# Performance work log

Hardware: AMD Instinct MI355X
Metric: run time of the kernel (lower is better)

Reference implementation:

```python
import jax, jax.numpy as jnp
import numpy as np

N_NODES = 50000
N_EDGES = 800000
IN_DIM = 128
HID = 64
ZDIM = 64
N_GRAPHS = 64


def gcn_conv(x, W, b, src, dst, n):
    # PyG GCNConv: add self-loops, symmetric deg^-1/2 normalization,
    # linear transform then gather-scatter aggregation.
    h = x @ W  # [N, out]
    loops = jnp.arange(n, dtype=src.dtype)
    s = jnp.concatenate([src, loops])
    d = jnp.concatenate([dst, loops])
    deg = jnp.zeros((n,), h.dtype).at[d].add(1.0)  # includes self-loops -> >=1
    dinv = jax.lax.rsqrt(deg)
    norm = dinv[s] * dinv[d]  # [E+N]
    msg = h[s] * norm[:, None]  # gather [E+N, out]
    out = jnp.zeros_like(h).at[d].add(msg)  # scatter-add
    return out + b


def mean_pool(h, batch, num_graphs):
    sums = jax.ops.segment_sum(h, batch, num_segments=num_graphs)
    cnt = jax.ops.segment_sum(jnp.ones((h.shape[0],), h.dtype), batch,
                              num_segments=num_graphs)
    return sums / jnp.maximum(cnt, 1.0)[:, None]


def setup_inputs() -> dict:
    key = jax.random.key(0)
    ks = jax.random.split(key, 9)
    x = jax.random.normal(ks[0], (N_NODES, IN_DIM), jnp.float32)
    edge_index = jax.random.randint(ks[1], (2, N_EDGES), 0, N_NODES, jnp.int64 if jax.config.jax_enable_x64 else jnp.int32)
    batch = jnp.sort(jax.random.randint(ks[2], (N_NODES,), 0, N_GRAPHS))
    s1 = 1.0 / np.sqrt(IN_DIM)
    s2 = 1.0 / np.sqrt(HID)
    W1 = jax.random.uniform(ks[3], (IN_DIM, HID), jnp.float32, -s1, s1)
    b1 = jnp.zeros((HID,), jnp.float32)
    Wmu = jax.random.uniform(ks[4], (HID, ZDIM), jnp.float32, -s2, s2)
    bmu = jnp.zeros((ZDIM,), jnp.float32)
    Wsig = jax.random.uniform(ks[5], (HID, ZDIM), jnp.float32, -s2, s2)
    bsig = jnp.zeros((ZDIM,), jnp.float32)
    return {"x": x, "edge_index": edge_index, "batch": batch,
            "num_graphs": N_GRAPHS, "W1": W1, "b1": b1,
            "Wmu": Wmu, "bmu": bmu, "Wsig": Wsig, "bsig": bsig}


def reference(x, edge_index, batch, num_graphs, W1, b1, Wmu, bmu, Wsig, bsig):
    src, dst = edge_index[0], edge_index[1]
    n = x.shape[0]
    h = jax.nn.elu(gcn_conv(x, W1, b1, src, dst, n))
    z_mu = mean_pool(jax.nn.elu(gcn_conv(h, Wmu, bmu, src, dst, n)), batch, num_graphs)
    z_sigma = mean_pool(jax.nn.elu(gcn_conv(h, Wsig, bsig, src, dst, n)), batch, num_graphs)
    return (z_mu, z_sigma)
```

## Files before the change

### kernel.cpp

```cpp
#include <hip/hip_runtime.h>
#include <hip/hip_fp16.h>


#define IN_DIM 128
#define HID 64
#define ZDIM 64
#define N_GRAPHS 64
#define SCAN_B 1024

typedef _Float16 half8 __attribute__((ext_vector_type(8)));
typedef float f32x4 __attribute__((ext_vector_type(4)));

__device__ __forceinline__ float elu1(float x) {
    return x > 0.f ? x : expm1f(x);
}

#define ACC8(RV, MV) do { \
    const __half2* _hp = (const __half2*)&(RV); \
    float2 _f0 = __half22float2(_hp[0]); \
    float2 _f1 = __half22float2(_hp[1]); \
    float2 _f2 = __half22float2(_hp[2]); \
    float2 _f3 = __half22float2(_hp[3]); \
    acc[0] = fmaf((MV), _f0.x, acc[0]); \
    acc[1] = fmaf((MV), _f0.y, acc[1]); \
    acc[2] = fmaf((MV), _f1.x, acc[2]); \
    acc[3] = fmaf((MV), _f1.y, acc[3]); \
    acc[4] = fmaf((MV), _f2.x, acc[4]); \
    acc[5] = fmaf((MV), _f2.y, acc[5]); \
    acc[6] = fmaf((MV), _f3.x, acc[6]); \
    acc[7] = fmaf((MV), _f3.y, acc[7]); \
  } while (0)

__global__ void k_count(const int* __restrict__ dst, int* __restrict__ kc,
                        int* __restrict__ rank, int E) {
    int e = blockIdx.x * blockDim.x + threadIdx.x;
    if (e < E) rank[e] = atomicAdd(&kc[dst[e]], 1);
}

__global__ __launch_bounds__(SCAN_B) void k_scan1(const int* __restrict__ kc,
                                                  int* __restrict__ bsum, int n) {
    __shared__ int wpart[16];
    int tid = threadIdx.x, lane = tid & 63, w = tid >> 6;
    int i = blockIdx.x * SCAN_B + tid;
    int v = (i < n) ? kc[i] : 0;
#pragma unroll
    for (int d = 1; d < 64; d <<= 1) v += __shfl_xor(v, d, 64);
    if (lane == 0) wpart[w] = v;
    __syncthreads();
    if (tid < 16) {
        int t = wpart[tid];
#pragma unroll
        for (int d = 1; d < 16; d <<= 1) t += __shfl_xor(t, d, 64);
        if (tid == 0) bsum[blockIdx.x] = t;
    }
}

__global__ __launch_bounds__(SCAN_B) void k_scan3(const int* __restrict__ kc,
                                                  const int* __restrict__ bsum,
                                                  int* __restrict__ offs,
                                                  float* __restrict__ dinv,
                                                  int n, int nb) {
    __shared__ int wsum[16];
    __shared__ int sbase;
    int tid = threadIdx.x, lane = tid & 63, w = tid >> 6;
    if (tid < 64) {
        int v = (tid < nb) ? bsum[tid] : 0;
        int s = v;
#pragma unroll
        for (int d = 1; d < 64; d <<= 1) {
            int u = __shfl_up(s, d, 64);
            if (tid >= d) s += u;
        }
        if (tid == blockIdx.x) sbase = s - v;
    }
    int i = blockIdx.x * SCAN_B + tid;
    int v = (i < n) ? kc[i] : 0;
    int s = v;
#pragma unroll
    for (int d = 1; d < 64; d <<= 1) {
        int u = __shfl_up(s, d, 64);
        if (lane >= d) s += u;
    }
    if (lane == 63) wsum[w] = s;
    __syncthreads();
    if (tid < 16) {
        int t = wsum[tid];
#pragma unroll
        for (int d = 1; d < 16; d <<= 1) {
            int u = __shfl_up(t, d, 64);
            if (tid >= d) t += u;
        }
        wsum[tid] = t;
    }
    __syncthreads();
    int base = sbase + ((w == 0) ? 0 : wsum[w - 1]);
    if (i < n) {
        offs[i + 1] = base + s;
        dinv[i] = 1.0f / sqrtf(1.0f + (float)v);
        if (i == 0) offs[0] = 0;
    }
}

__global__ void k_fill(const int* __restrict__ src, const int* __restrict__ dst,
                       const int* __restrict__ rank, const int* __restrict__ offs,
                       int* __restrict__ csr, int E) {
    int e = blockIdx.x * blockDim.x + threadIdx.x;
    if (e < E) csr[offs[dst[e]] + rank[e]] = src[e];
}

__global__ void k_wfrag(const float* __restrict__ W1,
                        const float* __restrict__ Wmu,
                        const float* __restrict__ Wsig,
                        __half* __restrict__ F1,
                        __half* __restrict__ Fmu,
                        __half* __restrict__ Fsig) {
    int e = blockIdx.x * 256 + threadIdx.x;
    if (e < 8192) {
        int j = e & 7, l = (e >> 3) & 63, ct = (e >> 9) & 3, ks = e >> 11;
        F1[e] = __float2half(W1[(ks * 32 + ((l >> 4) & 3) * 8 + j) * 64 + ct * 16 + (l & 15)]);
    }
    if (e < 4096) {
        int j = e & 7, l = (e >> 3) & 63, ct = (e >> 9) & 3, ks = e >> 11;
        int widx = (ks * 32 + ((l >> 4) & 3) * 8 + j) * 64 + ct * 16 + (l & 15);
        Fmu[e] = __float2half(Wmu[widx]);
        Fsig[e] = __float2half(Wsig[widx]);
    }
}

__global__ __launch_bounds__(256) void k_mm1(const float* __restrict__ x,
                                             const __half* __restrict__ F1,
                                             const float* __restrict__ dinv,
                                             __half* __restrict__ ts1h, int n) {
    int l = threadIdx.x & 63;
    int wave = threadIdx.x >> 6;
    int m0 = blockIdx.x * 64 + wave * 16;
    int row_a = m0 + (l & 15);
    if (row_a >= n) row_a = n - 1;
    int kg = l >> 4;

    f32x4 acc0 = {0.f, 0.f, 0.f, 0.f};
    f32x4 acc1 = acc0, acc2 = acc0, acc3 = acc0;

    const float* xr = x + (size_t)row_a * IN_DIM + kg * 8;
#pragma unroll
    for (int ks = 0; ks < 4; ++ks) {
        float4 xa = *(const float4*)(xr + ks * 32);
        float4 xb = *(const float4*)(xr + ks * 32 + 4);
        half8 a;
        a[0] = (_Float16)xa.x; a[1] = (_Float16)xa.y;
        a[2] = (_Float16)xa.z; a[3] = (_Float16)xa.w;
        a[4] = (_Float16)xb.x; a[5] = (_Float16)xb.y;
        a[6] = (_Float16)xb.z; a[7] = (_Float16)xb.w;
        const __half* fb = F1 + ((size_t)(ks * 4) * 64 + l) * 8;
        half8 b0 = *(const half8*)(fb);
        half8 b1 = *(const half8*)(fb + 512);
        half8 b2 = *(const half8*)(fb + 1024);
        half8 b3 = *(const half8*)(fb + 1536);
        acc0 = __builtin_amdgcn_mfma_f32_16x16x32_f16(a, b0, acc0, 0, 0, 0);
        acc1 = __builtin_amdgcn_mfma_f32_16x16x32_f16(a, b1, acc1, 0, 0, 0);
        acc2 = __builtin_amdgcn_mfma_f32_16x16x32_f16(a, b2, acc2, 0, 0, 0);
        acc3 = __builtin_amdgcn_mfma_f32_16x16x32_f16(a, b3, acc3, 0, 0, 0);
    }
    int col = l & 15;
#pragma unroll
    for (int r = 0; r < 4; ++r) {
        int row = m0 + kg * 4 + r;
        if (row < n) {
            float di = dinv[row];
            __half* p = &ts1h[(size_t)row * 64 + col];
            p[0]  = __float2half(acc0[r] * di);
            p[16] = __float2half(acc1[r] * di);
            p[32] = __float2half(acc2[r] * di);
            p[48] = __float2half(acc3[r] * di);
        }
    }
}

__global__ __launch_bounds__(256) void k_gather_hh(const int* __restrict__ off,
                                                   const int* __restrict__ csr,
                                                   const float* __restrict__ dinv,
                                                   const __half* __restrict__ ts,
                                                   const float* __restrict__ b1,
                                                   __half* __restrict__ hh, int n) {
    int node = blockIdx.x * 4 + (threadIdx.x >> 6);
    if (node >= n) return;
    int lane = threadIdx.x & 63;
    int g = lane >> 3, sub = lane & 7;
    int s0 = off[node], s1 = off[node + 1];
    float acc[8];
#pragma unroll
    for (int j = 0; j < 8; ++j) acc[j] = 0.f;

    if (s1 > s0) {
        int last = s1 - 1;
        int p0 = s0 + g, p1 = p0 + 8, p2 = p0 + 16, p3 = p0 + 24;
        int i0 = csr[p0 < s1 ? p0 : last];
        int i1 = csr[p1 < s1 ? p1 : last];
        int i2 = csr[p2 < s1 ? p2 : last];
        int i3 = csr[p3 < s1 ? p3 : last];
        float4 r0 = *(const float4*)&ts[(size_t)i0 * 64 + sub * 8];
        float4 r1 = *(const float4*)&ts[(size_t)i1 * 64 + sub * 8];
        float4 r2 = *(const float4*)&ts[(size_t)i2 * 64 + sub * 8];
        float4 r3 = *(const float4*)&ts[(size_t)i3 * 64 + sub * 8];
        float m0 = (p0 < s1) ? 1.f : 0.f;
        float m1 = (p1 < s1) ? 1.f : 0.f;
        float m2 = (p2 < s1) ? 1.f : 0.f;
        float m3 = (p3 < s1) ? 1.f : 0.f;
        ACC8(r0, m0);
        ACC8(r1, m1);
        ACC8(r2, m2);
        ACC8(r3, m3);
        for (int k = s0 + 32 + g; k < s1; k += 8) {
            int iv = csr[k];
            float4 rv = *(const float4*)&ts[(size_t)iv * 64 + sub * 8];
            ACC8(rv, 1.f);
        }
    }

#pragma unroll
    for (int j = 0; j < 8; ++j) {
        acc[j] += __shfl_xor(acc[j], 8, 64);
        acc[j] += __shfl_xor(acc[j], 16, 64);
        acc[j] += __shfl_xor(acc[j], 32, 64);
    }

    if (g == 0) {
        float4 sr = *(const float4*)&ts[(size_t)node * 64 + sub * 8];
        const __half2* sh = (const __half2*)&sr;
        float di = dinv[node];
        const float4* b4 = (const float4*)b1;
        float4 ba = b4[sub * 2], bb = b4[sub * 2 + 1];
        float2 f0 = __half22float2(sh[0]);
        float2 f1 = __half22float2(sh[1]);
        float2 f2 = __half22float2(sh[2]);
        float2 f3 = __half22float2(sh[3]);
        float e0 = elu1((acc[0] + f0.x) * di + ba.x) * di;
        float e1 = elu1((acc[1] + f0.y) * di + ba.y) * di;
        float e2 = elu1((acc[2] + f1.x) * di + ba.z) * di;
        float e3 = elu1((acc[3] + f1.y) * di + ba.w) * di;
        float e4 = elu1((acc[4] + f2.x) * di + bb.x) * di;
        float e5 = elu1((acc[5] + f2.y) * di + bb.y) * di;
        float e6 = elu1((acc[6] + f3.x) * di + bb.z) * di;
        float e7 = elu1((acc[7] + f3.y) * di + bb.w) * di;
        float4 outv;
        __half2* op = (__half2*)&outv;
        op[0] = __floats2half2_rn(e0, e1);
        op[1] = __floats2half2_rn(e2, e3);
        op[2] = __floats2half2_rn(e4, e5);
        op[3] = __floats2half2_rn(e6, e7);
        *(float4*)&hh[(size_t)node * 64 + sub * 8] = outv;
    }
}

__global__ __launch_bounds__(256) void k_gather_g(const int* __restrict__ off,
                                                  const int* __restrict__ csr,
                                                  const float* __restrict__ dinv,
                                                  const __half* __restrict__ hh,
                                                  float* __restrict__ gout, int n) {
    int node = blockIdx.x * 4 + (threadIdx.x >> 6);
    if (node >= n) return;
    int lane = threadIdx.x & 63;
    int g = lane >> 3, sub = lane & 7;
    int s0 = off[node], s1 = off[node + 1];
    float acc[8];
#pragma unroll
    for (int j = 0; j < 8; ++j) acc[j] = 0.f;

    if (s1 > s0) {
        int last = s1 - 1;
        int p0 = s0 + g, p1 = p0 + 8, p2 = p0 + 16, p3 = p0 + 24;
        int i0 = csr[p0 < s1 ? p0 : last];
        int i1 = csr[p1 < s1 ? p1 : last];
        int i2 = csr[p2 < s1 ? p2 : last];
        int i3 = csr[p3 < s1 ? p3 : last];
        float4 r0 = *(const float4*)&hh[(size_t)i0 * 64 + sub * 8];
        float4 r1 = *(const float4*)&hh[(size_t)i1 * 64 + sub * 8];
        float4 r2 = *(const float4*)&hh[(size_t)i2 * 64 + sub * 8];
        float4 r3 = *(const float4*)&hh[(size_t)i3 * 64 + sub * 8];
        float m0 = (p0 < s1) ? 1.f : 0.f;
        float m1 = (p1 < s1) ? 1.f : 0.f;
        float m2 = (p2 < s1) ? 1.f : 0.f;
        float m3 = (p3 < s1) ? 1.f : 0.f;
        ACC8(r0, m0);
        ACC8(r1, m1);
        ACC8(r2, m2);
        ACC8(r3, m3);
        for (int k = s0 + 32 + g; k < s1; k += 8) {
            int iv = csr[k];
            float4 rv = *(const float4*)&hh[(size_t)iv * 64 + sub * 8];
            ACC8(rv, 1.f);
        }
    }

#pragma unroll
    for (int j = 0; j < 8; ++j) {
        acc[j] += __shfl_xor(acc[j], 8, 64);
        acc[j] += __shfl_xor(acc[j], 16, 64);
        acc[j] += __shfl_xor(acc[j], 32, 64);
    }

    if (g == 0) {
        float4 sr = *(const float4*)&hh[(size_t)node * 64 + sub * 8];
        const __half2* sh = (const __half2*)&sr;
        float di = dinv[node];
        float2 f0 = __half22float2(sh[0]);
        float2 f1 = __half22float2(sh[1]);
        float2 f2 = __half22float2(sh[2]);
        float2 f3 = __half22float2(sh[3]);
        float o0 = (acc[0] + f0.x) * di;
        float o1 = (acc[1] + f0.y) * di;
        float o2 = (acc[2] + f1.x) * di;
        float o3 = (acc[3] + f1.y) * di;
        float o4 = (acc[4] + f2.x) * di;
        float o5 = (acc[5] + f2.y) * di;
        float o6 = (acc[6] + f3.x) * di;
        float o7 = (acc[7] + f3.y) * di;
        *(float4*)&gout[(size_t)node * 64 + sub * 8] = make_float4(o0, o1, o2, o3);
        *(float4*)&gout[(size_t)node * 64 + sub * 8 + 4] = make_float4(o4, o5, o6, o7);
    }
}

__global__ __launch_bounds__(256) void k_mm_pool(const float* __restrict__ g,
                                                 const __half* __restrict__ Fmu,
                                                 const __half* __restrict__ Fsig,
                                                 const float* __restrict__ bmu,
                                                 const float* __restrict__ bsig,
                                                 const int* __restrict__ batch,
                                                 float* __restrict__ sums, int n) {
    __shared__ float wc[64 * 132];
    __shared__ int bs[64];
    const int tid = threadIdx.x;
    int l = tid & 63, wave = tid >> 6;
    int m0 = blockIdx.x * 64;
    int row_a = m0 + wave * 16 + (l & 15);
    if (row_a >= n) row_a = n - 1;
    int kg = l >> 4;

    f32x4 am[4], as[4];
#pragma unroll
    for (int ct = 0; ct < 4; ++ct) {
        am[ct] = (f32x4){0.f, 0.f, 0.f, 0.f};
        as[ct] = (f32x4){0.f, 0.f, 0.f, 0.f};
    }

    const float* gr = g + (size_t)row_a * 64 + kg * 8;
#pragma unroll
    for (int ks = 0; ks < 2; ++ks) {
        float4 xa = *(const float4*)(gr + ks * 32);
        float4 xb = *(const float4*)(gr + ks * 32 + 4);
        half8 a;
        a[0] = (_Float16)xa.x; a[1] = (_Float16)xa.y;
        a[2] = (_Float16)xa.z; a[3] = (_Float16)xa.w;
        a[4] = (_Float16)xb.x; a[5] = (_Float16)xb.y;
        a[6] = (_Float16)xb.z; a[7] = (_Float16)xb.w;
        const __half* fm = Fmu + ((size_t)(ks * 4) * 64 + l) * 8;
        const __half* fs = Fsig + ((size_t)(ks * 4) * 64 + l) * 8;
#pragma unroll
        for (int ct = 0; ct < 4; ++ct) {
            half8 bm = *(const half8*)(fm + ct * 512);
            half8 bv = *(const half8*)(fs + ct * 512);
            am[ct] = __builtin_amdgcn_mfma_f32_16x16x32_f16(a, bm, am[ct], 0, 0, 0);
            as[ct] = __builtin_amdgcn_mfma_f32_16x16x32_f16(a, bv, as[ct], 0, 0, 0);
        }
    }

    if (tid < 64) bs[tid] = (m0 + tid < n) ? batch[m0 + tid] : -1;

    int col = l & 15;
#pragma unroll
    for (int ct = 0; ct < 4; ++ct) {
        float bM = bmu[ct * 16 + col];
        float bS = bsig[ct * 16 + col];
#pragma unroll
        for (int r = 0; r < 4; ++r) {
            int rr = wave * 16 + kg * 4 + r;
            wc[rr * 132 + ct * 16 + col] = elu1(am[ct][r] + bM);
            wc[rr * 132 + 64 + ct * 16 + col] = elu1(as[ct][r] + bS);
        }
    }
    __syncthreads();

    int d = tid & 127, seg = tid >> 7;
    int base = (d < 64) ? d : (64 * 64 - 64 + d);
    float acc = 0.f;
    int gcur = -1;
    int r0 = seg * 32;
    for (int r = r0; r < r0 + 32; ++r) {
        int gb = bs[r];
        if (gb < 0) break;
        float v = wc[r * 132 + d];
        if (gb != gcur) {
            if (gcur >= 0) atomicAdd(&sums[base + gcur * 64], acc);
            acc = 0.f;
            gcur = gb;
        }
        acc += v;
    }
    if (gcur >= 0) atomicAdd(&sums[base + gcur * 64], acc);
}

__global__ void k_pool_final(const float* __restrict__ sums,
                             const int* __restrict__ batch,
                             float* __restrict__ out, int n) {
    int i = blockIdx.x * blockDim.x + threadIdx.x;
    if (i >= 2 * N_GRAPHS * ZDIM) return;
    int g = (i >> 6) & 63;
    int lo = 0, hi = n;
    while (lo < hi) { int m = (lo + hi) >> 1; if (batch[m] < g) lo = m + 1; else hi = m; }
    int s = lo;
    lo = s; hi = n;
    while (lo < hi) { int m = (lo + hi) >> 1; if (batch[m] < g + 1) lo = m + 1; else hi = m; }
    float c = fmaxf((float)(lo - s), 1.0f);
    out[i] = sums[i] / c;
}

extern "C" void kernel_launch(void* const* d_in, const int* in_sizes, int n_in,
                              void* d_out, int out_size, void* d_ws, size_t ws_size,
                              hipStream_t stream) {
    const float* x    = (const float*)d_in[0];
    const int*   ei   = (const int*)d_in[1];
    const int*   batch= (const int*)d_in[2];
    const float* W1   = (const float*)d_in[4];
    const float* b1   = (const float*)d_in[5];
    const float* Wmu  = (const float*)d_in[6];
    const float* bmu  = (const float*)d_in[7];
    const float* Wsig = (const float*)d_in[8];
    const float* bsig = (const float*)d_in[9];
    float* out = (float*)d_out;

    const int n = in_sizes[0] / IN_DIM;
    const int E = in_sizes[1] / 2;
    const int* src = ei;
    const int* dst = ei + E;
    const int NSB = (n + SCAN_B - 1) / SCAN_B;

    float* ws = (float*)d_ws;
    size_t off_w = 0;
    int*   kc   = (int*)(ws + off_w); off_w += 50048;
    float* sums = ws + off_w; off_w += 8192;
    float* dinv = ws + off_w; off_w += 50048;
    int*   offs = (int*)(ws + off_w); off_w += 50056;
    int*   bsum = (int*)(ws + off_w); off_w += 64;
    int*   rank = (int*)(ws + off_w); off_w += 800000;
    int*   csr  = (int*)(ws + off_w); off_w += 800000;
    off_w = (off_w + 15) & ~(size_t)15;
    __half* F1   = (__half*)(ws + off_w); off_w += 4096;
    __half* Fmu  = (__half*)(ws + off_w); off_w += 2048;
    __half* Fsig = (__half*)(ws + off_w); off_w += 2048;
    const size_t BIG = (size_t)n * 64;
    __half* ts1h = (__half*)(ws + off_w); off_w += BIG / 2;
    __half* hh   = (__half*)(ws + off_w); off_w += BIG / 2;
    float*  gbuf = ws + off_w; off_w += BIG;

    const int gE  = (E + 255) / 256;
    const int gNW = (n + 3) / 4;
    const int NB  = (n + 63) / 64;

    hipMemsetAsync(kc, 0, (50048 + 8192) * sizeof(int), stream);
    k_wfrag<<<32, 256, 0, stream>>>(W1, Wmu, Wsig, F1, Fmu, Fsig);
    k_count<<<gE, 256, 0, stream>>>(dst, kc, rank, E);
    k_scan1<<<NSB, SCAN_B, 0, stream>>>(kc, bsum, n);
    k_scan3<<<NSB, SCAN_B, 0, stream>>>(kc, bsum, offs, dinv, n, NSB);
    k_fill<<<gE, 256, 0, stream>>>(src, dst, rank, offs, csr, E);

    k_mm1<<<NB, 256, 0, stream>>>(x, F1, dinv, ts1h, n);
    k_gather_hh<<<gNW, 256, 0, stream>>>(offs, csr, dinv, ts1h, b1, hh, n);

    k_gather_g<<<gNW, 256, 0, stream>>>(offs, csr, dinv, hh, gbuf, n);

    k_mm_pool<<<NB, 256, 0, stream>>>(gbuf, Fmu, Fsig, bmu, bsig, batch, sums, n);
    k_pool_final<<<(2 * N_GRAPHS * ZDIM + 255) / 256, 256, 0, stream>>>(sums, batch, out, n);
}
```

Before: 220.2 us.

## Merge independent kernels via block-range dispatch and store aggregated layer-2 features in fp16

Weight-fragment packing is folded into the edge-count kernel, and the CSR fill is folded into the first matmul kernel, using block-index ranges, which removes two launches and lets independent work run concurrently. The layer-2 aggregation output is now written as fp16 instead of fp32, halving that intermediate's write and read traffic. The pooled matmul loads half8 directly instead of converting from floats. The fp16 rounding point is unchanged because the values were already converted to fp16 before the MFMA.

```diff
diff --git a/kernel.cpp b/kernel.cpp
--- a/kernel.cpp
+++ b/kernel.cpp
@@ -31,10 +31,32 @@
     acc[7] = fmaf((MV), _f3.y, acc[7]); \
   } while (0)
 
-__global__ void k_count(const int* __restrict__ dst, int* __restrict__ kc,
-                        int* __restrict__ rank, int E) {
-    int e = blockIdx.x * blockDim.x + threadIdx.x;
-    if (e < E) rank[e] = atomicAdd(&kc[dst[e]], 1);
+__global__ __launch_bounds__(256) void k_count_wfrag(const int* __restrict__ dst,
+                                                     int* __restrict__ kc,
+                                                     int* __restrict__ rank, int E,
+                                                     const float* __restrict__ W1,
+                                                     const float* __restrict__ Wmu,
+                                                     const float* __restrict__ Wsig,
+                                                     __half* __restrict__ F1,
+                                                     __half* __restrict__ Fmu,
+                                                     __half* __restrict__ Fsig,
+                                                     int fillBlocks) {
+    if ((int)blockIdx.x < fillBlocks) {
+        int e = blockIdx.x * 256 + threadIdx.x;
+        if (e < E) rank[e] = atomicAdd(&kc[dst[e]], 1);
+        return;
+    }
+    int e = (blockIdx.x - fillBlocks) * 256 + threadIdx.x;
+    if (e < 8192) {
+        int j = e & 7, l = (e >> 3) & 63, ct = (e >> 9) & 3, ks = e >> 11;
+        F1[e] = __float2half(W1[(ks * 32 + ((l >> 4) & 3) * 8 + j) * 64 + ct * 16 + (l & 15)]);
+    }
+    if (e < 4096) {
+        int j = e & 7, l = (e >> 3) & 63, ct = (e >> 9) & 3, ks = e >> 11;
+        int widx = (ks * 32 + ((l >> 4) & 3) * 8 + j) * 64 + ct * 16 + (l & 15);
+        Fmu[e] = __float2half(Wmu[widx]);
+        Fsig[e] = __float2half(Wsig[widx]);
+    }
 }
 
 __global__ __launch_bounds__(SCAN_B) void k_scan1(const int* __restrict__ kc,
@@ -101,39 +123,25 @@
     }
 }
 
-__global__ void k_fill(const int* __restrict__ src, const int* __restrict__ dst,
-                       const int* __restrict__ rank, const int* __restrict__ offs,
-                       int* __restrict__ csr, int E) {
-    int e = blockIdx.x * blockDim.x + threadIdx.x;
-    if (e < E) csr[offs[dst[e]] + rank[e]] = src[e];
-}
-
-__global__ void k_wfrag(const float* __restrict__ W1,
-                        const float* __restrict__ Wmu,
-                        const float* __restrict__ Wsig,
-                        __half* __restrict__ F1,
-                        __half* __restrict__ Fmu,
-                        __half* __restrict__ Fsig) {
-    int e = blockIdx.x * 256 + threadIdx.x;
-    if (e < 8192) {
-        int j = e & 7, l = (e >> 3) & 63, ct = (e >> 9) & 3, ks = e >> 11;
-        F1[e] = __float2half(W1[(ks * 32 + ((l >> 4) & 3) * 8 + j) * 64 + ct * 16 + (l & 15)]);
-    }
-    if (e < 4096) {
-        int j = e & 7, l = (e >> 3) & 63, ct = (e >> 9) & 3, ks = e >> 11;
-        int widx = (ks * 32 + ((l >> 4) & 3) * 8 + j) * 64 + ct * 16 + (l & 15);
-        Fmu[e] = __float2half(Wmu[widx]);
-        Fsig[e] = __float2half(Wsig[widx]);
-    }
-}
-
-__global__ __launch_bounds__(256) void k_mm1(const float* __restrict__ x,
-                                             const __half* __restrict__ F1,
-                                             const float* __restrict__ dinv,
-                                             __half* __restrict__ ts1h, int n) {
+__global__ __launch_bounds__(256) void k_fill_mm1(const int* __restrict__ src,
+                                                  const int* __restrict__ dst,
+                                                  const int* __restrict__ rank,
+                                                  const int* __restrict__ offs,
+                                                  int* __restrict__ csr, int E,
+                                                  const float* __restrict__ x,
+                                                  const __half* __restrict__ F1,
+                                                  const float* __restrict__ dinv,
+                                                  __half* __restrict__ ts1h, int n,
+                                                  int fillBlocks) {
+    if ((int)blockIdx.x < fillBlocks) {
+        int e = blockIdx.x * 256 + threadIdx.x;
+        if (e < E) csr[offs[dst[e]] + rank[e]] = src[e];
+        return;
+    }
+    int bid = blockIdx.x - fillBlocks;
     int l = threadIdx.x & 63;
     int wave = threadIdx.x >> 6;
-    int m0 = blockIdx.x * 64 + wave * 16;
+    int m0 = bid * 64 + wave * 16;
     int row_a = m0 + (l & 15);
     if (row_a >= n) row_a = n - 1;
     int kg = l >> 4;
@@ -256,7 +264,7 @@
                                                   const int* __restrict__ csr,
                                                   const float* __restrict__ dinv,
                                                   const __half* __restrict__ hh,
-                                                  float* __restrict__ gout, int n) {
+                                                  __half* __restrict__ gh2, int n) {
     int node = blockIdx.x * 4 + (threadIdx.x >> 6);
     if (node >= n) return;
     int lane = threadIdx.x & 63;
@@ -307,20 +315,17 @@
         float2 f1 = __half22float2(sh[1]);
         float2 f2 = __half22float2(sh[2]);
         float2 f3 = __half22float2(sh[3]);
-        float o0 = (acc[0] + f0.x) * di;
-        float o1 = (acc[1] + f0.y) * di;
-        float o2 = (acc[2] + f1.x) * di;
-        float o3 = (acc[3] + f1.y) * di;
-        float o4 = (acc[4] + f2.x) * di;
-        float o5 = (acc[5] + f2.y) * di;
-        float o6 = (acc[6] + f3.x) * di;
-        float o7 = (acc[7] + f3.y) * di;
-        *(float4*)&gout[(size_t)node * 64 + sub * 8] = make_float4(o0, o1, o2, o3);
-        *(float4*)&gout[(size_t)node * 64 + sub * 8 + 4] = make_float4(o4, o5, o6, o7);
-    }
-}
-
-__global__ __launch_bounds__(256) void k_mm_pool(const float* __restrict__ g,
+        float4 outv;
+        __half2* op = (__half2*)&outv;
+        op[0] = __floats2half2_rn((acc[0] + f0.x) * di, (acc[1] + f0.y) * di);
+        op[1] = __floats2half2_rn((acc[2] + f1.x) * di, (acc[3] + f1.y) * di);
+        op[2] = __floats2half2_rn((acc[4] + f2.x) * di, (acc[5] + f2.y) * di);
+        op[3] = __floats2half2_rn((acc[6] + f3.x) * di, (acc[7] + f3.y) * di);
+        *(float4*)&gh2[(size_t)node * 64 + sub * 8] = outv;
+    }
+}
+
+__global__ __launch_bounds__(256) void k_mm_pool(const __half* __restrict__ gh2,
                                                  const __half* __restrict__ Fmu,
                                                  const __half* __restrict__ Fsig,
                                                  const float* __restrict__ bmu,
@@ -343,16 +348,10 @@
         as[ct] = (f32x4){0.f, 0.f, 0.f, 0.f};
     }
 
-    const float* gr = g + (size_t)row_a * 64 + kg * 8;
+    const __half* gr = gh2 + (size_t)row_a * 64 + kg * 8;
 #pragma unroll
     for (int ks = 0; ks < 2; ++ks) {
-        float4 xa = *(const float4*)(gr + ks * 32);
-        float4 xb = *(const float4*)(gr + ks * 32 + 4);
-        half8 a;
-        a[0] = (_Float16)xa.x; a[1] = (_Float16)xa.y;
-        a[2] = (_Float16)xa.z; a[3] = (_Float16)xa.w;
-        a[4] = (_Float16)xb.x; a[5] = (_Float16)xb.y;
-        a[6] = (_Float16)xb.z; a[7] = (_Float16)xb.w;
+        half8 a = *(const half8*)(gr + ks * 32);
         const __half* fm = Fmu + ((size_t)(ks * 4) * 64 + l) * 8;
         const __half* fs = Fsig + ((size_t)(ks * 4) * 64 + l) * 8;
 #pragma unroll
@@ -450,24 +449,25 @@
     const size_t BIG = (size_t)n * 64;
     __half* ts1h = (__half*)(ws + off_w); off_w += BIG / 2;
     __half* hh   = (__half*)(ws + off_w); off_w += BIG / 2;
-    float*  gbuf = ws + off_w; off_w += BIG;
+    __half* gh2  = (__half*)(ws + off_w); off_w += BIG / 2;
 
     const int gE  = (E + 255) / 256;
     const int gNW = (n + 3) / 4;
     const int NB  = (n + 63) / 64;
 
     hipMemsetAsync(kc, 0, (50048 + 8192) * sizeof(int), stream);
-    k_wfrag<<<32, 256, 0, stream>>>(W1, Wmu, Wsig, F1, Fmu, Fsig);
-    k_count<<<gE, 256, 0, stream>>>(dst, kc, rank, E);
+    k_count_wfrag<<<gE + 32, 256, 0, stream>>>(dst, kc, rank, E,
+                                               W1, Wmu, Wsig, F1, Fmu, Fsig, gE);
     k_scan1<<<NSB, SCAN_B, 0, stream>>>(kc, bsum, n);
     k_scan3<<<NSB, SCAN_B, 0, stream>>>(kc, bsum, offs, dinv, n, NSB);
-    k_fill<<<gE, 256, 0, stream>>>(src, dst, rank, offs, csr, E);
-
-    k_mm1<<<NB, 256, 0, stream>>>(x, F1, dinv, ts1h, n);
+
+    k_fill_mm1<<<gE + NB, 256, 0, stream>>>(src, dst, rank, offs, csr, E,
+                                            x, F1, dinv, ts1h, n, gE);
+
     k_gather_hh<<<gNW, 256, 0, stream>>>(offs, csr, dinv, ts1h, b1, hh, n);
 
-    k_gather_g<<<gNW, 256, 0, stream>>>(offs, csr, dinv, hh, gbuf, n);
-
-    k_mm_pool<<<NB, 256, 0, stream>>>(gbuf, Fmu, Fsig, bmu, bsig, batch, sums, n);
+    k_gather_g<<<gNW, 256, 0, stream>>>(offs, csr, dinv, hh, gh2, n);
+
+    k_mm_pool<<<NB, 256, 0, stream>>>(gh2, Fmu, Fsig, bmu, bsig, batch, sums, n);
     k_pool_final<<<(2 * N_GRAPHS * ZDIM + 255) / 256, 256, 0, stream>>>(sums, batch, out, n);
 }
```

New measurement: 217.1 us. About the same (-1.4%).
